# Performance work log

Measured on AMD Instinct MI355X. Metric: run time of the kernel, lower is better.

Reference implementation:

```python
import jax, jax.numpy as jnp
import numpy as np


def _layernorm(x, g, b, eps=1e-5):
    m = x.mean(-1, keepdims=True)
    v = ((x - m) ** 2).mean(-1, keepdims=True)
    return (x - m) * jax.lax.rsqrt(v + eps) * g + b


def _silu(x):
    return x * jax.nn.sigmoid(x)


def _mamba_mixer(x, in_w, conv_w, conv_b, xp_w, dt_w, dt_b, A_log, Dp, out_w):
    # x: (B, L, C) ; HF Mamba slow-path math
    B, L, C = x.shape
    dI = in_w.shape[0] // 2
    h, gate = jnp.split(x @ in_w.T, 2, axis=-1)  # (B, L, dI) each
    hc = jnp.transpose(h, (0, 2, 1))             # (B, dI, L)
    K = conv_w.shape[-1]
    hc = jax.lax.conv_general_dilated(hc, conv_w, (1,), [(K - 1, 0)],
                                      feature_group_count=dI,
                                      dimension_numbers=('NCH', 'OIH', 'NCH'))
    hc = _silu(hc + conv_b[None, :, None])
    u = jnp.transpose(hc, (0, 2, 1))             # (B, L, dI)
    R = dt_w.shape[1]
    N = A_log.shape[1]
    dt, Bs, Cs = jnp.split(u @ xp_w.T, [R, R + N], axis=-1)
    dt = jax.nn.softplus(dt @ dt_w.T + dt_b)     # (B, L, dI)
    A = -jnp.exp(A_log)                          # (dI, N)
    dA = jnp.exp(dt[..., None] * A)              # (B, L, dI, N)
    dBu = dt[..., None] * Bs[:, :, None, :] * u[..., None]  # (B, L, dI, N)

    def step(state, inp):
        dA_t, dBu_t, C_t = inp
        state = dA_t * state + dBu_t             # (B, dI, N)
        y = jnp.einsum('bdn,bn->bd', state, C_t)
        return state, y

    h0 = jnp.zeros((B, dI, N), x.dtype)
    _, ys = jax.lax.scan(step, h0, (jnp.swapaxes(dA, 0, 1),
                                    jnp.swapaxes(dBu, 0, 1),
                                    jnp.swapaxes(Cs, 0, 1)))
    y = jnp.swapaxes(ys, 0, 1)                   # (B, L, dI)
    y = (y + u * Dp) * _silu(gate)
    return y @ out_w.T


def _mixffn(x, H, W, fc1_w, fc1_b, pe_w, pe_b, fc2_w, fc2_b):
    B, L, C = x.shape
    img = jnp.transpose(x, (0, 2, 1)).reshape(B, C, H, W)
    t = jnp.einsum('bchw,fc->bfhw', img, fc1_w[:, :, 0, 0]) + fc1_b[None, :, None, None]
    Fch = pe_w.shape[0]
    t = jax.lax.conv_general_dilated(t, pe_w, (1, 1), [(1, 1), (1, 1)],
                                     feature_group_count=Fch,
                                     dimension_numbers=('NCHW', 'OIHW', 'NCHW'))
    t = t + pe_b[None, :, None, None]
    t = jax.nn.gelu(t, approximate=False)
    t = jnp.einsum('bfhw,cf->bchw', t, fc2_w[:, :, 0, 0]) + fc2_b[None, :, None, None]
    return jnp.transpose(t.reshape(B, C, L), (0, 2, 1))


def _forward(x, norm1_g, norm1_b, in_w, conv_w, conv_b, xp_w, dt_w, dt_b, A_log, Dp,
             out_w, norm2_g, norm2_b, gate_w, fc1_w, fc1_b, pe_w, pe_b, fc2_w, fc2_b,
             rand_index, H, W):
    identity = x
    B = x.shape[0]
    x_in = jnp.concatenate([x, jnp.flip(x, 1), x[:, rand_index]], axis=0)  # (3B, L, C)
    xn = _layernorm(x_in, norm1_g, norm1_b)
    y = _mamba_mixer(xn, in_w, conv_w, conv_b, xp_w, dt_w, dt_b, A_log, Dp, out_w)
    fwd, rev, shf = jnp.split(y, 3, axis=0)
    rev = jnp.flip(rev, 1)
    inv = jnp.argsort(rand_index)
    shf = shf[:, inv]
    g_in = jnp.concatenate([fwd.mean(1), rev.mean(1), shf.mean(1)], axis=-1)  # (B, 3C)
    g = jax.nn.softmax(g_in @ gate_w.T, axis=-1)                              # (B, 3)
    y = g[:, 0, None, None] * fwd + g[:, 1, None, None] * rev + g[:, 2, None, None] * shf
    x1 = identity + y
    xn2 = _layernorm(x1, norm2_g, norm2_b)
    return x1 + _mixffn(xn2, H, W, fc1_w, fc1_b, pe_w, pe_b, fc2_w, fc2_b)


def setup_inputs() -> dict:
    B, H, W, C = 2, 64, 64, 128
    L = H * W
    dI, N, K, R, Fch = 384, 4, 4, 128, 512
    key = jax.random.key(0)
    ks = jax.random.split(key, 32)
    s = lambda i, shape, sc=0.02: jax.random.normal(ks[i], shape, jnp.float32) * sc
    A_log = jnp.log(jnp.broadcast_to(jnp.arange(1, N + 1, dtype=jnp.float32), (dI, N)))
    return {
        'x': jax.random.normal(ks[0], (B, L, C), jnp.float32),
        'rand_index': jax.random.permutation(ks[1], L),
        'H': H, 'W': W,
        'norm1_g': jnp.ones((C,), jnp.float32),
        'norm1_b': jnp.zeros((C,), jnp.float32),
        'in_w': s(2, (2 * dI, C)),
        'conv_w': s(3, (dI, 1, K), 0.1),
        'conv_b': jnp.zeros((dI,), jnp.float32),
        'xp_w': s(4, (R + 2 * N, dI)),
        'dt_w': s(5, (dI, R)),
        'dt_b': s(6, (dI,), 0.1),
        'A_log': A_log,
        'Dp': jnp.ones((dI,), jnp.float32),
        'out_w': s(7, (C, dI)),
        'norm2_g': jnp.ones((C,), jnp.float32),
        'norm2_b': jnp.zeros((C,), jnp.float32),
        'gate_w': s(8, (3, 3 * C)),
        'fc1_w': s(9, (Fch, C, 1, 1)),
        'fc1_b': jnp.zeros((Fch,), jnp.float32),
        'pe_w': s(10, (Fch, 1, 3, 3), 0.1),
        'pe_b': jnp.zeros((Fch,), jnp.float32),
        'fc2_w': s(11, (C, Fch, 1, 1)),
        'fc2_b': jnp.zeros((C,), jnp.float32),
    }


def reference(x, rand_index, H, W, norm1_g, norm1_b, in_w, conv_w, conv_b, xp_w,
              dt_w, dt_b, A_log, Dp, out_w, norm2_g, norm2_b, gate_w,
              fc1_w, fc1_b, pe_w, pe_b, fc2_w, fc2_b):
    return _forward(x, norm1_g, norm1_b, in_w, conv_w, conv_b, xp_w, dt_w, dt_b,
                    A_log, Dp, out_w, norm2_g, norm2_b, gate_w, fc1_w, fc1_b,
                    pe_w, pe_b, fc2_w, fc2_b, rand_index, H, W)
```

## Files before the change

kernel.cpp:

```cpp
#include <hip/hip_runtime.h>
#include <math.h>

#define LLEN 4096
#define CCH 128
#define DI 384
#define NST 4
#define SBN 6
#define NB 2
#define FCH 512
#define NCHUNK 128
#define TSTEP 32

typedef short bf16x8 __attribute__((ext_vector_type(8)));
typedef short bf16x4 __attribute__((ext_vector_type(4)));
typedef float f32x4 __attribute__((ext_vector_type(4)));
typedef float f32x8 __attribute__((ext_vector_type(8)));

__device__ __forceinline__ float wave_sum(float v) {
#pragma unroll
    for (int o = 32; o > 0; o >>= 1) v += __shfl_xor(v, o);
    return v;
}

__device__ __forceinline__ short f2bf(float f) {
    unsigned int u = __float_as_uint(f);
    unsigned int r = (u + 0x7fffu + ((u >> 16) & 1u)) >> 16;
    return (short)r;
}
__device__ __forceinline__ float bf2f(short s) {
    return __uint_as_float(((unsigned int)(unsigned short)s) << 16);
}

#define OFF_IN  0
#define OFF_DTC 98304
#define OFF_BC  245760
#define OFF_OUT 248832
#define OFF_FC1 297984
#define OFF_FC2 363520
#define OFF_END 429056
#define NCONV   281600
#define NCBLK   1100
#define GWCBLK  14
#define LN1OFF  (NCBLK + 576 + GWCBLK + 16)
#define LN1BLK  2048

__global__ __launch_bounds__(256) void conv_comp(const float* __restrict__ in_w,
                                                 const float* __restrict__ xp_w,
                                                 const float* __restrict__ dt_w,
                                                 const float* __restrict__ out_w,
                                                 const float* __restrict__ fc1_w,
                                                 const float* __restrict__ fc2_w,
                                                 const float* __restrict__ gate_w,
                                                 const int* __restrict__ ridx,
                                                 const float* __restrict__ x,
                                                 const float* __restrict__ n1g,
                                                 const float* __restrict__ n1b,
                                                 short* __restrict__ wb,
                                                 float* __restrict__ colsum,
                                                 float* __restrict__ gwc,
                                                 int* __restrict__ inv,
                                                 short* __restrict__ xn)
{
    int bid = blockIdx.x;
    if (bid < NCBLK) {
        int i = bid * 256 + threadIdx.x;
        if (i >= NCONV) return;
        int idx = (i < OFF_DTC) ? i : i + (OFF_OUT - OFF_DTC);
        float v;
        if (idx < OFF_DTC)      v = in_w[idx];
        else if (idx < OFF_OUT) v = xp_w[128 * 384 + (idx - OFF_BC)];
        else if (idx < OFF_FC1) v = out_w[idx - OFF_OUT];
        else if (idx < OFF_FC2) v = fc1_w[idx - OFF_FC1];
        else                    v = fc2_w[idx - OFF_FC2];
        wb[idx] = f2bf(v);
    } else if (bid < NCBLK + 576) {
        if (bid == NCBLK) {
            for (int i = threadIdx.x; i < SBN * DI; i += 256) colsum[i] = 0.f;
        }
        int ji = (bid - NCBLK) * 256 + threadIdx.x;
        int j = ji / 384, k = ji % 384;
        float acc = 0.f;
#pragma unroll 8
        for (int n = 0; n < 128; n++)
            acc += dt_w[j * 128 + n] * xp_w[n * 384 + k];
        wb[OFF_DTC + j * 384 + k] = f2bf(acc);
    } else if (bid < NCBLK + 576 + GWCBLK) {
        int idx = (bid - NCBLK - 576) * 256 + threadIdx.x;
        if (idx >= 3456) return;
        int j = idx / 1152, rem = idx % 1152;
        int s = rem / 384, d = rem % 384;
        float acc = 0.f;
#pragma unroll 8
        for (int c = 0; c < 128; c++)
            acc += gate_w[j * 384 + s * 128 + c] * out_w[c * 384 + d];
        gwc[idx] = acc;
    } else if (bid < LN1OFF) {
        int l = (bid - NCBLK - 576 - GWCBLK) * 256 + threadIdx.x;
        if (l < LLEN) inv[ridx[l]] = l;
    } else {
        int r = (bid - LN1OFF) * 4 + (threadIdx.x >> 6);
        int lane = threadIdx.x & 63;
        const float* src = x + (size_t)r * CCH;
        float v0 = src[lane], v1 = src[lane + 64];
        float m = wave_sum(v0 + v1) * (1.f / 128.f);
        float d0 = v0 - m, d1 = v1 - m;
        float var = wave_sum(d0 * d0 + d1 * d1) * (1.f / 128.f);
        float rstd = rsqrtf(var + 1e-5f);
        short* dst = xn + (size_t)r * CCH;
        dst[lane]      = f2bf(d0 * rstd * n1g[lane]      + n1b[lane]);
        dst[lane + 64] = f2bf(d1 * rstd * n1g[lane + 64] + n1b[lane + 64]);
    }
}

template<int EPI>
__global__ __launch_bounds__(256) void gemm_w(const short* __restrict__ A, int lda,
                                              const short* __restrict__ W, int ldw,
                                              const float* __restrict__ bias,
                                              short* __restrict__ Cb, int ldc,
                                              int Kd)
{
    __shared__ short Als[64 * 72];
    __shared__ short Wls[128 * 72];
    int tid = threadIdx.x;
    int wid = tid >> 6, lane = tid & 63;
    int wm = wid >> 1, wn = wid & 1;
    int l15 = lane & 15, l4 = lane >> 4;
    int bm = blockIdx.x * 64, bn = blockIdx.y * 128;
    int srow = tid >> 3, scol = (tid & 7) * 8;
    f32x4 acc[2][4] = {};
    for (int k0 = 0; k0 < Kd; k0 += 64) {
        bf16x8 av0 = *(const bf16x8*)&A[(size_t)(bm + srow) * lda + k0 + scol];
        bf16x8 av1 = *(const bf16x8*)&A[(size_t)(bm + srow + 32) * lda + k0 + scol];
        bf16x8 wv[4];
#pragma unroll
        for (int q = 0; q < 4; q++)
            wv[q] = *(const bf16x8*)&W[(size_t)(bn + srow + 32 * q) * ldw + k0 + scol];
        __syncthreads();
        *(bf16x8*)&Als[srow * 72 + scol] = av0;
        *(bf16x8*)&Als[(srow + 32) * 72 + scol] = av1;
#pragma unroll
        for (int q = 0; q < 4; q++)
            *(bf16x8*)&Wls[(srow + 32 * q) * 72 + scol] = wv[q];
        __syncthreads();
#pragma unroll
        for (int ks = 0; ks < 2; ks++) {
            bf16x8 af[2], bw[4];
#pragma unroll
            for (int f = 0; f < 2; f++)
                af[f] = *(const bf16x8*)&Als[(wm * 32 + f * 16 + l15) * 72 + ks * 32 + l4 * 8];
#pragma unroll
            for (int j = 0; j < 4; j++)
                bw[j] = *(const bf16x8*)&Wls[(wn * 64 + j * 16 + l15) * 72 + ks * 32 + l4 * 8];
#pragma unroll
            for (int i = 0; i < 2; i++)
#pragma unroll
                for (int j = 0; j < 4; j++)
                    acc[i][j] = __builtin_amdgcn_mfma_f32_16x16x32_bf16(af[i], bw[j], acc[i][j], 0, 0, 0);
        }
    }
#pragma unroll
    for (int i = 0; i < 2; i++) {
        int row0 = bm + wm * 32 + i * 16 + l4 * 4;
#pragma unroll
        for (int j = 0; j < 4; j++) {
            int col = bn + wn * 64 + j * 16 + l15;
            float bv = (EPI == 6) ? bias[col] : 0.f;
#pragma unroll
            for (int r = 0; r < 4; r++)
                Cb[(size_t)(row0 + r) * ldc + col] = f2bf(acc[i][j][r] + bv);
        }
    }
}

__global__ __launch_bounds__(256) void gemm_bc(const short* __restrict__ A,
                                               const short* __restrict__ W,
                                               float* __restrict__ C0)
{
    __shared__ short Als[64 * 72];
    __shared__ short Wls[64 * 72];
    int tid = threadIdx.x;
    int wid = tid >> 6, lane = tid & 63;
    int wm = wid >> 1, wn = wid & 1;
    int l15 = lane & 15, l4 = lane >> 4;
    int bm = blockIdx.x * 64;
    int srow = tid >> 3, scol = (tid & 7) * 8;
    f32x4 acc[2][2] = {};
    for (int k0 = 0; k0 < DI; k0 += 64) {
        bf16x8 av0 = *(const bf16x8*)&A[(size_t)(bm + srow) * DI + k0 + scol];
        bf16x8 av1 = *(const bf16x8*)&A[(size_t)(bm + srow + 32) * DI + k0 + scol];
        bf16x8 wv0 = {};
        if (srow < 8) wv0 = *(const bf16x8*)&W[(size_t)srow * DI + k0 + scol];
        __syncthreads();
        *(bf16x8*)&Als[srow * 72 + scol] = av0;
        *(bf16x8*)&Als[(srow + 32) * 72 + scol] = av1;
        *(bf16x8*)&Wls[srow * 72 + scol] = wv0;
        if (srow >= 24) *(bf16x8*)&Wls[(srow + 32) * 72 + scol] = bf16x8{};
        else if (srow >= 8) *(bf16x8*)&Wls[srow * 72 + scol] = wv0;
        __syncthreads();
#pragma unroll
        for (int ks = 0; ks < 2; ks++) {
            bf16x8 af[2];
#pragma unroll
            for (int f = 0; f < 2; f++)
                af[f] = *(const bf16x8*)&Als[(wm * 32 + f * 16 + l15) * 72 + ks * 32 + l4 * 8];
            if (wn == 0) {
                bf16x8 bw = *(const bf16x8*)&Wls[(l15)*72 + ks * 32 + l4 * 8];
#pragma unroll
                for (int i = 0; i < 2; i++)
                    acc[i][0] = __builtin_amdgcn_mfma_f32_16x16x32_bf16(af[i], bw, acc[i][0], 0, 0, 0);
            }
        }
    }
    if (wn == 0 && l15 < 8) {
#pragma unroll
        for (int i = 0; i < 2; i++) {
            int row0 = bm + wm * 32 + i * 16 + l4 * 4;
#pragma unroll
            for (int r = 0; r < 4; r++)
                C0[(size_t)(row0 + r) * 8 + l15] = acc[i][0][r];
        }
    }
}

__global__ __launch_bounds__(256) void gemm_dt(const short* __restrict__ A,
                                               const short* __restrict__ W,
                                               const float* __restrict__ bias,
                                               short* __restrict__ Cb)
{
    __shared__ short Als[64 * 72];
    __shared__ short Wls[384 * 72];
    int tid = threadIdx.x;
    int wid = tid >> 6, lane = tid & 63;
    int wm = wid >> 1, wn = wid & 1;
    int l15 = lane & 15, l4 = lane >> 4;
    int bm = blockIdx.x * 64;
    int srow = tid >> 3, scol = (tid & 7) * 8;
    f32x4 acc[2][12] = {};
    for (int k0 = 0; k0 < 384; k0 += 64) {
        bf16x8 av0 = *(const bf16x8*)&A[(size_t)(bm + srow) * DI + k0 + scol];
        bf16x8 av1 = *(const bf16x8*)&A[(size_t)(bm + srow + 32) * DI + k0 + scol];
        bf16x8 wv[12];
#pragma unroll
        for (int q = 0; q < 12; q++)
            wv[q] = *(const bf16x8*)&W[(size_t)(srow + 32 * q) * DI + k0 + scol];
        __syncthreads();
        *(bf16x8*)&Als[srow * 72 + scol] = av0;
        *(bf16x8*)&Als[(srow + 32) * 72 + scol] = av1;
#pragma unroll
        for (int q = 0; q < 12; q++)
            *(bf16x8*)&Wls[(srow + 32 * q) * 72 + scol] = wv[q];
        __syncthreads();
#pragma unroll
        for (int ks = 0; ks < 2; ks++) {
            bf16x8 af[2];
#pragma unroll
            for (int f = 0; f < 2; f++)
                af[f] = *(const bf16x8*)&Als[(wm * 32 + f * 16 + l15) * 72 + ks * 32 + l4 * 8];
#pragma unroll
            for (int j = 0; j < 12; j++) {
                bf16x8 bw = *(const bf16x8*)&Wls[(wn * 192 + j * 16 + l15) * 72 + ks * 32 + l4 * 8];
#pragma unroll
                for (int i = 0; i < 2; i++)
                    acc[i][j] = __builtin_amdgcn_mfma_f32_16x16x32_bf16(af[i], bw, acc[i][j], 0, 0, 0);
            }
        }
    }
#pragma unroll
    for (int i = 0; i < 2; i++) {
        int row0 = bm + wm * 32 + i * 16 + l4 * 4;
#pragma unroll
        for (int j = 0; j < 12; j++) {
            int col = wn * 192 + j * 16 + l15;
            float bv = bias[col];
#pragma unroll
            for (int r = 0; r < 4; r++) {
                float v = acc[i][j][r] + bv;
                v = (v > 20.f) ? v : __logf(1.f + __expf(v));
                Cb[(size_t)(row0 + r) * DI + col] = f2bf(v);
            }
        }
    }
}

__global__ __launch_bounds__(192) void dwconv_silu_v3(const short* __restrict__ hg,
                                                      const int* __restrict__ ridx,
                                                      const float* __restrict__ cw,
                                                      const float* __restrict__ cb,
                                                      short* __restrict__ ub)
{
    int t = threadIdx.x;
    int c = t % 48, rs = t / 48;
    int blk = blockIdx.x;
    int sb = blk >> 7;
    int s = sb >> 1, bb = sb & 1;
    int l0 = ((blk & 127) << 5) + rs * 8;
    int d0 = c * 8;
    float w0[8], w1[8], w2[8], w3[8], bs[8];
#pragma unroll
    for (int e = 0; e < 8; e++) {
        int d = d0 + e;
        bs[e] = cb[d];
        w0[e] = cw[d * 4 + 0]; w1[e] = cw[d * 4 + 1];
        w2[e] = cw[d * 4 + 2]; w3[e] = cw[d * 4 + 3];
    }
    float r0[8], r1[8], r2[8];
#pragma unroll
    for (int e = 0; e < 8; e++) { r0[e] = 0.f; r1[e] = 0.f; r2[e] = 0.f; }
    if (l0 - 3 >= 0) {
        int j = l0 - 3;
        int sl = (s == 0) ? j : (s == 1 ? LLEN - 1 - j : ridx[j]);
        bf16x8 v = *(const bf16x8*)&hg[(size_t)(bb * LLEN + sl) * 768 + d0];
#pragma unroll
        for (int e = 0; e < 8; e++) r0[e] = bf2f(v[e]);
    }
    if (l0 - 2 >= 0) {
        int j = l0 - 2;
        int sl = (s == 0) ? j : (s == 1 ? LLEN - 1 - j : ridx[j]);
        bf16x8 v = *(const bf16x8*)&hg[(size_t)(bb * LLEN + sl) * 768 + d0];
#pragma unroll
        for (int e = 0; e < 8; e++) r1[e] = bf2f(v[e]);
    }
    if (l0 - 1 >= 0) {
        int j = l0 - 1;
        int sl = (s == 0) ? j : (s == 1 ? LLEN - 1 - j : ridx[j]);
        bf16x8 v = *(const bf16x8*)&hg[(size_t)(bb * LLEN + sl) * 768 + d0];
#pragma unroll
        for (int e = 0; e < 8; e++) r2[e] = bf2f(v[e]);
    }
#pragma unroll
    for (int i = 0; i < 8; i++) {
        int j = l0 + i;
        int sl = (s == 0) ? j : (s == 1 ? LLEN - 1 - j : ridx[j]);
        bf16x8 v = *(const bf16x8*)&hg[(size_t)(bb * LLEN + sl) * 768 + d0];
        float r3[8];
#pragma unroll
        for (int e = 0; e < 8; e++) r3[e] = bf2f(v[e]);
        bf16x8 ov;
#pragma unroll
        for (int e = 0; e < 8; e++) {
            float a = bs[e] + w0[e] * r0[e] + w1[e] * r1[e] + w2[e] * r2[e] + w3[e] * r3[e];
            ov[e] = f2bf(a * __builtin_amdgcn_rcpf(1.f + __expf(-a)));
        }
        *(bf16x8*)&ub[(size_t)(sb * LLEN + j) * DI + d0] = ov;
#pragma unroll
        for (int e = 0; e < 8; e++) { r0[e] = r1[e]; r1[e] = r2[e]; r2[e] = r3[e]; }
    }
}

__global__ __launch_bounds__(DI) void scan_phaseA2(const short* __restrict__ dtb,
                                                   const float* __restrict__ bc,
                                                   const short* __restrict__ ub,
                                                   const float* __restrict__ A_log,
                                                   float* __restrict__ PS)
{
    __shared__ short ds_dt[TSTEP * DI];
    __shared__ short ds_u[TSTEP * DI];
    __shared__ float ds_bc[TSTEP * 8];
    int tid = threadIdx.x;
    int bid = blockIdx.x;
    int sb = bid / NCHUNK, chunk = bid % NCHUNK;
    int base = sb * LLEN + chunk * TSTEP;
    {
        int rr = tid / 48, cc = (tid % 48) * 8;
#pragma unroll
        for (int p = 0; p < 4; p++) {
            int row = p * 8 + rr;
            *(bf16x8*)&ds_dt[row * DI + cc] = *(const bf16x8*)&dtb[(size_t)(base + row) * DI + cc];
            *(bf16x8*)&ds_u[row * DI + cc]  = *(const bf16x8*)&ub[(size_t)(base + row) * DI + cc];
        }
        if (tid < TSTEP * 8) ds_bc[tid] = bc[(size_t)base * 8 + tid];
    }
    int d = tid;
    f32x4 al = *(const f32x4*)&A_log[d * 4];
    float a[NST];
#pragma unroll
    for (int n = 0; n < NST; n++) a[n] = -__expf(al[n]);
    __syncthreads();
    float s[NST] = {0.f, 0.f, 0.f, 0.f}, p[NST] = {1.f, 1.f, 1.f, 1.f};
    for (int t = 0; t < TSTEP; t++) {
        float dtv = bf2f(ds_dt[t * DI + d]);
        float dtu = dtv * bf2f(ds_u[t * DI + d]);
#pragma unroll
        for (int n = 0; n < NST; n++) {
            float dA = __expf(dtv * a[n]);
            s[n] = dA * s[n] + dtu * ds_bc[t * 8 + n];
            p[n] *= dA;
        }
    }
    f32x8 v;
#pragma unroll
    for (int n = 0; n < NST; n++) { v[2 * n] = p[n]; v[2 * n + 1] = s[n]; }
    *(f32x8*)&PS[(size_t)(sb * NCHUNK + chunk) * 3072 + d * 8] = v;
}

__global__ __launch_bounds__(256) void scan_phaseB2(const float* __restrict__ PS,
                                                    float* __restrict__ I)
{
    int gid = blockIdx.x * 256 + threadIdx.x;
    if (gid >= SBN * 1536) return;
    int sb = gid / 1536, dn = gid % 1536;
    const float* ps = PS + (size_t)sb * NCHUNK * 3072 + dn * 2;
    float* Ip = I + (size_t)sb * NCHUNK * 1536 + dn;
    float st = 0.f;
    for (int c = 0; c < NCHUNK; c += 8) {
        float2 v[8];
#pragma unroll
        for (int q = 0; q < 8; q++) v[q] = *(const float2*)&ps[(size_t)(c + q) * 3072];
#pragma unroll
        for (int q = 0; q < 8; q++) { Ip[(size_t)(c + q) * 1536] = st; st = v[q].x * st + v[q].y; }
    }
}

__global__ __launch_bounds__(DI) void scan_phaseC3(const short* __restrict__ dtb,
                                                   const float* __restrict__ bc,
                                                   const short* __restrict__ ub,
                                                   const short* __restrict__ hg,
                                                   const int* __restrict__ ridx,
                                                   const float* __restrict__ A_log,
                                                   const float* __restrict__ Dp,
                                                   const float* __restrict__ I,
                                                   short* __restrict__ ymix,
                                                   float* __restrict__ colsum)
{
    __shared__ short ds_dt[TSTEP * DI];
    __shared__ short ds_u[TSTEP * DI];
    __shared__ float ds_bc[TSTEP * 8];
    __shared__ int ds_src[TSTEP];
    int tid = threadIdx.x;
    int bid = blockIdx.x;
    int sb = bid / NCHUNK, chunk = bid % NCHUNK;
    int s2 = sb >> 1, bb = sb & 1;
    int base = sb * LLEN + chunk * TSTEP;
    {
        int rr = tid / 48, cc = (tid % 48) * 8;
#pragma unroll
        for (int p = 0; p < 4; p++) {
            int row = p * 8 + rr;
            *(bf16x8*)&ds_dt[row * DI + cc] = *(const bf16x8*)&dtb[(size_t)(base + row) * DI + cc];
            *(bf16x8*)&ds_u[row * DI + cc]  = *(const bf16x8*)&ub[(size_t)(base + row) * DI + cc];
        }
        if (tid < TSTEP * 8) ds_bc[tid] = bc[(size_t)base * 8 + tid];
        if (tid < TSTEP) {
            int l = chunk * TSTEP + tid;
            int sl = (s2 == 0) ? l : (s2 == 1 ? LLEN - 1 - l : ridx[l]);
            ds_src[tid] = bb * LLEN + sl;
        }
    }
    int d = tid;
    f32x4 al = *(const f32x4*)&A_log[d * 4];
    float a[NST];
#pragma unroll
    for (int n = 0; n < NST; n++) a[n] = -__expf(al[n]);
    __syncthreads();
    float s[NST];
    {
        f32x4 si = *(const f32x4*)&I[(size_t)(sb * NCHUNK + chunk) * 1536 + d * 4];
#pragma unroll
        for (int n = 0; n < NST; n++) s[n] = si[n];
    }
    float Dv = Dp[d];
    float csum = 0.f;
    for (int t = 0; t < TSTEP; t++) {
        float dtv = bf2f(ds_dt[t * DI + d]);
        float uv = bf2f(ds_u[t * DI + d]);
        float dtu = dtv * uv;
        float y = 0.f;
#pragma unroll
        for (int n = 0; n < NST; n++) {
            float dA = __expf(dtv * a[n]);
            s[n] = dA * s[n] + dtu * ds_bc[t * 8 + n];
            y += s[n] * ds_bc[t * 8 + 4 + n];
        }
        float gt = bf2f(hg[(size_t)ds_src[t] * 768 + 384 + d]);
        float sg = gt * __builtin_amdgcn_rcpf(1.f + __expf(-gt));
        float val = (y + uv * Dv) * sg;
        ymix[(size_t)(base + t) * DI + d] = f2bf(val);
        csum += val;
    }
    atomicAdd(&colsum[sb * DI + d], csum);
}

__global__ __launch_bounds__(256) void combine_outproj_ln2(const short* __restrict__ ymix,
                                                           const float* __restrict__ x,
                                                           const float* __restrict__ colsum,
                                                           const float* __restrict__ gwc,
                                                           const int* __restrict__ inv,
                                                           const short* __restrict__ Wout,
                                                           const float* __restrict__ n2g,
                                                           const float* __restrict__ n2b,
                                                           float* __restrict__ x1,
                                                           short* __restrict__ xn2)
{
    __shared__ short Als[64 * 72];
    __shared__ short Wls[128 * 72];
    __shared__ float xs[64][132];
    __shared__ int ssrc[192];
    __shared__ float msh[64], rsh[64];
    __shared__ float part[4][3];
    __shared__ float gsh[3];
    int tid = threadIdx.x;
    int bm = blockIdx.x * 64;
    int bb = bm >> 12;
    if (tid < 64) {
        int l = (bm & 4095) + tid;
        ssrc[tid * 3 + 0] = bb * LLEN + l;
        ssrc[tid * 3 + 1] = (2 + bb) * LLEN + (LLEN - 1 - l);
        ssrc[tid * 3 + 2] = (4 + bb) * LLEN + inv[l];
    }
    int wid = tid >> 6, lane = tid & 63;
    {
        float a0 = 0.f, a1 = 0.f, a2 = 0.f;
        for (int i = tid; i < 1152; i += 256) {
            int s = i / 384, d = i % 384;
            float cv = colsum[(s * 2 + bb) * 384 + d];
            a0 += cv * gwc[i];
            a1 += cv * gwc[1152 + i];
            a2 += cv * gwc[2304 + i];
        }
        a0 = wave_sum(a0); a1 = wave_sum(a1); a2 = wave_sum(a2);
        if (lane == 0) { part[wid][0] = a0; part[wid][1] = a1; part[wid][2] = a2; }
    }
    __syncthreads();
    if (tid == 0) {
        float l0 = 0.f, l1 = 0.f, l2 = 0.f;
#pragma unroll
        for (int w = 0; w < 4; w++) { l0 += part[w][0]; l1 += part[w][1]; l2 += part[w][2]; }
        l0 *= (1.f / 4096.f); l1 *= (1.f / 4096.f); l2 *= (1.f / 4096.f);
        float mx = fmaxf(l0, fmaxf(l1, l2));
        float e0 = __expf(l0 - mx), e1 = __expf(l1 - mx), e2 = __expf(l2 - mx);
        float iv = __builtin_amdgcn_rcpf(e0 + e1 + e2);
        gsh[0] = e0 * iv; gsh[1] = e1 * iv; gsh[2] = e2 * iv;
    }
    __syncthreads();
    float g0 = gsh[0], g1 = gsh[1], g2 = gsh[2];
    int wm = wid >> 1, wn = wid & 1;
    int l15 = lane & 15, l4 = lane >> 4;
    int srow = tid >> 3, scol = (tid & 7) * 8;
    f32x4 acc[2][4] = {};
    for (int k0 = 0; k0 < DI; k0 += 64) {
        bf16x8 cmb[2];
#pragma unroll
        for (int hh = 0; hh < 2; hh++) {
            int r = srow + 32 * hh;
            bf16x8 vf = *(const bf16x8*)&ymix[(size_t)ssrc[r * 3 + 0] * DI + k0 + scol];
            bf16x8 vr = *(const bf16x8*)&ymix[(size_t)ssrc[r * 3 + 1] * DI + k0 + scol];
            bf16x8 vs = *(const bf16x8*)&ymix[(size_t)ssrc[r * 3 + 2] * DI + k0 + scol];
#pragma unroll
            for (int e = 0; e < 8; e++)
                cmb[hh][e] = f2bf(g0 * bf2f(vf[e]) + g1 * bf2f(vr[e]) + g2 * bf2f(vs[e]));
        }
        bf16x8 wv[4];
#pragma unroll
        for (int q = 0; q < 4; q++)
            wv[q] = *(const bf16x8*)&Wout[(size_t)(srow + 32 * q) * DI + k0 + scol];
        __syncthreads();
        *(bf16x8*)&Als[srow * 72 + scol] = cmb[0];
        *(bf16x8*)&Als[(srow + 32) * 72 + scol] = cmb[1];
#pragma unroll
        for (int q = 0; q < 4; q++)
            *(bf16x8*)&Wls[(srow + 32 * q) * 72 + scol] = wv[q];
        __syncthreads();
#pragma unroll
        for (int ks = 0; ks < 2; ks++) {
            bf16x8 af[2], bw[4];
#pragma unroll
            for (int f = 0; f < 2; f++)
                af[f] = *(const bf16x8*)&Als[(wm * 32 + f * 16 + l15) * 72 + ks * 32 + l4 * 8];
#pragma unroll
            for (int j = 0; j < 4; j++)
                bw[j] = *(const bf16x8*)&Wls[(wn * 64 + j * 16 + l15) * 72 + ks * 32 + l4 * 8];
#pragma unroll
            for (int i = 0; i < 2; i++)
#pragma unroll
                for (int j = 0; j < 4; j++)
                    acc[i][j] = __builtin_amdgcn_mfma_f32_16x16x32_bf16(af[i], bw[j], acc[i][j], 0, 0, 0);
        }
    }
#pragma unroll
    for (int i = 0; i < 2; i++) {
        int rowl = wm * 32 + i * 16 + l4 * 4;
#pragma unroll
        for (int j = 0; j < 4; j++) {
            int col = wn * 64 + j * 16 + l15;
#pragma unroll
            for (int r = 0; r < 4; r++)
                xs[rowl + r][col] = acc[i][j][r] + x[(size_t)(bm + rowl + r) * CCH + col];
        }
    }
    __syncthreads();
    {
        int row = tid >> 2, q = tid & 3;
        float sum = 0.f, sq = 0.f;
#pragma unroll
        for (int c = q * 32; c < q * 32 + 32; c++) { float v = xs[row][c]; sum += v; sq += v * v; }
        sum += __shfl_xor(sum, 1); sq += __shfl_xor(sq, 1);
        sum += __shfl_xor(sum, 2); sq += __shfl_xor(sq, 2);
        if (q == 0) {
            float m = sum * (1.f / 128.f);
            float var = sq * (1.f / 128.f) - m * m;
            msh[row] = m;
            rsh[row] = rsqrtf(fmaxf(var, 0.f) + 1e-5f);
        }
    }
    __syncthreads();
    {
        int col = tid & 127;
        float gg = n2g[col], b2 = n2b[col];
#pragma unroll
        for (int e = 0; e < 32; e++) {
            int row = e * 2 + (tid >> 7);
            float v = xs[row][col];
            x1[(size_t)(bm + row) * CCH + col] = v;
            xn2[(size_t)(bm + row) * CCH + col] = f2bf((v - msh[row]) * rsh[row] * gg + b2);
        }
    }
}

__global__ __launch_bounds__(256) void peconv_fc2(const short* __restrict__ t,
                                                  const float* __restrict__ pw,
                                                  const float* __restrict__ pb,
                                                  const short* __restrict__ W2,
                                                  const float* __restrict__ fc2_b,
                                                  const float* __restrict__ x1,
                                                  float* __restrict__ out)
{
    __shared__ short t2ls[32 * 520];
    __shared__ short Wls[128 * 72];
    int tid = threadIdx.x;
    int fc = tid & 127;
    int wsr = tid >> 7;
    int blk = blockIdx.x;
    int whalf = blk & 1, h = (blk >> 1) & 63, bb = blk >> 7;
    int w0 = whalf * 32 + wsr * 16;
    int f0 = fc * 4;
    {
        float wt[9][4], bias4[4];
#pragma unroll
        for (int e = 0; e < 4; e++) {
            bias4[e] = pb[f0 + e];
#pragma unroll
            for (int k = 0; k < 9; k++) wt[k][e] = pw[(f0 + e) * 9 + k];
        }
        size_t base = (size_t)bb * 4096 * FCH;
        float cm1[3][4], cc[3][4], cn[3][4];
#pragma unroll
        for (int rr = 0; rr < 3; rr++)
#pragma unroll
            for (int e = 0; e < 4; e++) { cm1[rr][e] = 0.f; cc[rr][e] = 0.f; }
#pragma unroll
        for (int rr = 0; rr < 3; rr++) {
            int hh = h + rr - 1;
            if (hh >= 0 && hh < 64) {
                if (w0 - 1 >= 0) {
                    bf16x4 v = *(const bf16x4*)&t[base + ((size_t)hh * 64 + (w0 - 1)) * FCH + f0];
#pragma unroll
                    for (int e = 0; e < 4; e++) cm1[rr][e] = bf2f(v[e]);
                }
                bf16x4 v = *(const bf16x4*)&t[base + ((size_t)hh * 64 + w0) * FCH + f0];
#pragma unroll
                for (int e = 0; e < 4; e++) cc[rr][e] = bf2f(v[e]);
            }
        }
#pragma unroll
        for (int i = 0; i < 16; i++) {
            int w = w0 + i;
#pragma unroll
            for (int rr = 0; rr < 3; rr++) {
#pragma unroll
                for (int e = 0; e < 4; e++) cn[rr][e] = 0.f;
                int hh = h + rr - 1;
                if (hh >= 0 && hh < 64 && w + 1 < 64) {
                    bf16x4 v = *(const bf16x4*)&t[base + ((size_t)hh * 64 + (w + 1)) * FCH + f0];
#pragma unroll
                    for (int e = 0; e < 4; e++) cn[rr][e] = bf2f(v[e]);
                }
            }
            bf16x4 ov;
#pragma unroll
            for (int e = 0; e < 4; e++) {
                float acc = bias4[e];
#pragma unroll
                for (int rr = 0; rr < 3; rr++) {
                    acc += wt[rr * 3 + 0][e] * cm1[rr][e];
                    acc += wt[rr * 3 + 1][e] * cc[rr][e];
                    acc += wt[rr * 3 + 2][e] * cn[rr][e];
                }
                ov[e] = f2bf(0.5f * acc * (1.f + erff(acc * 0.70710678118654752f)));
            }
            int pix = wsr * 16 + i;
            *(bf16x4*)&t2ls[pix * 520 + f0] = ov;
#pragma unroll
            for (int rr = 0; rr < 3; rr++)
#pragma unroll
                for (int e = 0; e < 4; e++) { cm1[rr][e] = cc[rr][e]; cc[rr][e] = cn[rr][e]; }
        }
    }
    __syncthreads();
    int wid = tid >> 6, lane = tid & 63;
    int wm = wid >> 1, wn = wid & 1;
    int l15 = lane & 15, l4 = lane >> 4;
    int srow = tid >> 3, scol = (tid & 7) * 8;
    int bm = bb * 4096 + h * 64 + whalf * 32;
    f32x4 acc[4] = {};
    for (int k0 = 0; k0 < FCH; k0 += 64) {
        bf16x8 wv[4];
#pragma unroll
        for (int q = 0; q < 4; q++)
            wv[q] = *(const bf16x8*)&W2[(size_t)(srow + 32 * q) * FCH + k0 + scol];
        __syncthreads();
#pragma unroll
        for (int q = 0; q < 4; q++)
            *(bf16x8*)&Wls[(srow + 32 * q) * 72 + scol] = wv[q];
        __syncthreads();
#pragma unroll
        for (int ks = 0; ks < 2; ks++) {
            bf16x8 af = *(const bf16x8*)&t2ls[(wm * 16 + l15) * 520 + k0 + ks * 32 + l4 * 8];
#pragma unroll
            for (int j = 0; j < 4; j++) {
                bf16x8 bw = *(const bf16x8*)&Wls[(wn * 64 + j * 16 + l15) * 72 + ks * 32 + l4 * 8];
                acc[j] = __builtin_amdgcn_mfma_f32_16x16x32_bf16(af, bw, acc[j], 0, 0, 0);
            }
        }
    }
#pragma unroll
    for (int j = 0; j < 4; j++) {
        int col = wn * 64 + j * 16 + l15;
        float bv = fc2_b[col];
#pragma unroll
        for (int r = 0; r < 4; r++) {
            int row = bm + wm * 16 + l4 * 4 + r;
            out[(size_t)row * CCH + col] = acc[j][r] + bv + x1[(size_t)row * CCH + col];
        }
    }
}

extern "C" void kernel_launch(void* const* d_in, const int* in_sizes, int n_in,
                              void* d_out, int out_size, void* d_ws, size_t ws_size,
                              hipStream_t stream)
{
    (void)in_sizes; (void)n_in; (void)ws_size; (void)out_size;
    const float* x      = (const float*)d_in[0];
    const int*   ridx   = (const int*)d_in[1];
    const float* n1g    = (const float*)d_in[4];
    const float* n1b    = (const float*)d_in[5];
    const float* in_w   = (const float*)d_in[6];
    const float* conv_w = (const float*)d_in[7];
    const float* conv_b = (const float*)d_in[8];
    const float* xp_w   = (const float*)d_in[9];
    const float* dt_w   = (const float*)d_in[10];
    const float* dt_b   = (const float*)d_in[11];
    const float* A_log  = (const float*)d_in[12];
    const float* Dp     = (const float*)d_in[13];
    const float* out_w  = (const float*)d_in[14];
    const float* n2g    = (const float*)d_in[15];
    const float* n2b    = (const float*)d_in[16];
    const float* gate_w = (const float*)d_in[17];
    const float* fc1_w  = (const float*)d_in[18];
    const float* fc1_b  = (const float*)d_in[19];
    const float* pe_w   = (const float*)d_in[20];
    const float* pe_b   = (const float*)d_in[21];
    const float* fc2_w  = (const float*)d_in[22];
    const float* fc2_b  = (const float*)d_in[23];
    float* out = (float*)d_out;

    float* ws = (float*)d_ws;
    short* wb   = (short*)ws;
    float* regA = ws + 215040;
    float* regB = regA + 2097152;
    float* regC = regB + 9437184;
    float* regD = regC + 4718592;
    float* regE = regD + 4718592;
    float* regF = regE + 4718592;
    float* regG = regF + 2359296;
    float* smallb = regG + 196608;

    short* xn   = (short*)regA;
    float* Ibuf = regA;
    short* tbuf = (short*)regA;
    short* hg   = (short*)regB;
    float* x1   = regB + 3145728;
    short* xn2  = (short*)(regB + 4194304);
    short* ub   = (short*)regC;
    short* ymix = (short*)regD;
    short* dtb  = (short*)regE;
    float* PS   = regF;
    float* xpbc = regG;
    float* colsum = smallb;
    float* gwcb   = smallb + 2304;
    float* gbuf   = gwcb + 3456;
    int*   invb   = (int*)(gbuf + 8);
    (void)gbuf;

    const int M6 = SBN * LLEN;
    const int M2 = NB * LLEN;

    conv_comp<<<LN1OFF + LN1BLK, 256, 0, stream>>>(in_w, xp_w, dt_w, out_w, fc1_w, fc2_w,
                                                   gate_w, ridx, x, n1g, n1b,
                                                   wb, colsum, gwcb, invb, xn);
    gemm_w<5><<<dim3(M2 / 64, 6), 256, 0, stream>>>(xn, CCH, wb + OFF_IN, CCH, nullptr, hg, 768, CCH);
    dwconv_silu_v3<<<768, 192, 0, stream>>>(hg, ridx, conv_w, conv_b, ub);
    gemm_bc<<<M6 / 64, 256, 0, stream>>>(ub, wb + OFF_BC, xpbc);
    gemm_dt<<<M6 / 64, 256, 0, stream>>>(ub, wb + OFF_DTC, dt_b, dtb);
    scan_phaseA2<<<SBN * NCHUNK, DI, 0, stream>>>(dtb, xpbc, ub, A_log, PS);
    scan_phaseB2<<<36, 256, 0, stream>>>(PS, Ibuf);
    scan_phaseC3<<<SBN * NCHUNK, DI, 0, stream>>>(dtb, xpbc, ub, hg, ridx, A_log, Dp, Ibuf, ymix, colsum);
    combine_outproj_ln2<<<M2 / 64, 256, 0, stream>>>(ymix, x, colsum, gwcb, invb, wb + OFF_OUT, n2g, n2b, x1, xn2);
    gemm_w<6><<<dim3(M2 / 64, 4), 256, 0, stream>>>(xn2, CCH, wb + OFF_FC1, CCH, fc1_b, tbuf, FCH, CCH);
    peconv_fc2<<<256, 256, 0, stream>>>(tbuf, pe_w, pe_b, wb + OFF_FC2, fc2_b, x1, out);
}
```

Baseline: 172.7 us.

## Fuse dt and B/C projections into one GEMM; fuse fc1 into out-proj/LN2 kernel

The separate gemm_bc and gemm_dt kernels become a single gemm_dtbc. It reads the ub activation once and handles the 8 B/C columns as an extra 16-column MFMA tile on the wn==1 waves. It assumes the B/C weight rows sit directly after the dt weight rows at OFF_DTC+384*DI. The fc1 GEMM is also folded into combine_outproj_ln2: the LN2 output is staged in shared memory and multiplied by W1 in-kernel, so the xn2 round trip and two launches go away. In exchange, the merged projection kernel uses more shared memory and registers, and the combine kernel now runs four serial 128-column fc1 tiles with only 128 blocks, which may lower parallelism.

Measured after the change: 170.7 us. No clear change (-1.2%).

```diff
diff --git a/kernel.cpp b/kernel.cpp
--- a/kernel.cpp
+++ b/kernel.cpp
@@ -172,70 +172,21 @@
     }
 }
 
-__global__ __launch_bounds__(256) void gemm_bc(const short* __restrict__ A,
-                                               const short* __restrict__ W,
-                                               float* __restrict__ C0)
+__global__ __launch_bounds__(256) void gemm_dtbc(const short* __restrict__ A,
+                                                 const short* __restrict__ W,
+                                                 const float* __restrict__ bias,
+                                                 short* __restrict__ Cb,
+                                                 float* __restrict__ bcout)
 {
     __shared__ short Als[64 * 72];
-    __shared__ short Wls[64 * 72];
+    __shared__ short Wls[400 * 72];
     int tid = threadIdx.x;
     int wid = tid >> 6, lane = tid & 63;
     int wm = wid >> 1, wn = wid & 1;
     int l15 = lane & 15, l4 = lane >> 4;
     int bm = blockIdx.x * 64;
     int srow = tid >> 3, scol = (tid & 7) * 8;
-    f32x4 acc[2][2] = {};
-    for (int k0 = 0; k0 < DI; k0 += 64) {
-        bf16x8 av0 = *(const bf16x8*)&A[(size_t)(bm + srow) * DI + k0 + scol];
-        bf16x8 av1 = *(const bf16x8*)&A[(size_t)(bm + srow + 32) * DI + k0 + scol];
-        bf16x8 wv0 = {};
-        if (srow < 8) wv0 = *(const bf16x8*)&W[(size_t)srow * DI + k0 + scol];
-        __syncthreads();
-        *(bf16x8*)&Als[srow * 72 + scol] = av0;
-        *(bf16x8*)&Als[(srow + 32) * 72 + scol] = av1;
-        *(bf16x8*)&Wls[srow * 72 + scol] = wv0;
-        if (srow >= 24) *(bf16x8*)&Wls[(srow + 32) * 72 + scol] = bf16x8{};
-        else if (srow >= 8) *(bf16x8*)&Wls[srow * 72 + scol] = wv0;
-        __syncthreads();
-#pragma unroll
-        for (int ks = 0; ks < 2; ks++) {
-            bf16x8 af[2];
-#pragma unroll
-            for (int f = 0; f < 2; f++)
-                af[f] = *(const bf16x8*)&Als[(wm * 32 + f * 16 + l15) * 72 + ks * 32 + l4 * 8];
-            if (wn == 0) {
-                bf16x8 bw = *(const bf16x8*)&Wls[(l15)*72 + ks * 32 + l4 * 8];
-#pragma unroll
-                for (int i = 0; i < 2; i++)
-                    acc[i][0] = __builtin_amdgcn_mfma_f32_16x16x32_bf16(af[i], bw, acc[i][0], 0, 0, 0);
-            }
-        }
-    }
-    if (wn == 0 && l15 < 8) {
-#pragma unroll
-        for (int i = 0; i < 2; i++) {
-            int row0 = bm + wm * 32 + i * 16 + l4 * 4;
-#pragma unroll
-            for (int r = 0; r < 4; r++)
-                C0[(size_t)(row0 + r) * 8 + l15] = acc[i][0][r];
-        }
-    }
-}
-
-__global__ __launch_bounds__(256) void gemm_dt(const short* __restrict__ A,
-                                               const short* __restrict__ W,
-                                               const float* __restrict__ bias,
-                                               short* __restrict__ Cb)
-{
-    __shared__ short Als[64 * 72];
-    __shared__ short Wls[384 * 72];
-    int tid = threadIdx.x;
-    int wid = tid >> 6, lane = tid & 63;
-    int wm = wid >> 1, wn = wid & 1;
-    int l15 = lane & 15, l4 = lane >> 4;
-    int bm = blockIdx.x * 64;
-    int srow = tid >> 3, scol = (tid & 7) * 8;
-    f32x4 acc[2][12] = {};
+    f32x4 acc[2][13] = {};
     for (int k0 = 0; k0 < 384; k0 += 64) {
         bf16x8 av0 = *(const bf16x8*)&A[(size_t)(bm + srow) * DI + k0 + scol];
         bf16x8 av1 = *(const bf16x8*)&A[(size_t)(bm + srow + 32) * DI + k0 + scol];
@@ -243,12 +194,16 @@
 #pragma unroll
         for (int q = 0; q < 12; q++)
             wv[q] = *(const bf16x8*)&W[(size_t)(srow + 32 * q) * DI + k0 + scol];
+        bf16x8 wbc = {};
+        if (srow < 8) wbc = *(const bf16x8*)&W[(size_t)(384 + srow) * DI + k0 + scol];
         __syncthreads();
         *(bf16x8*)&Als[srow * 72 + scol] = av0;
         *(bf16x8*)&Als[(srow + 32) * 72 + scol] = av1;
 #pragma unroll
         for (int q = 0; q < 12; q++)
             *(bf16x8*)&Wls[(srow + 32 * q) * 72 + scol] = wv[q];
+        if (srow < 16)
+            *(bf16x8*)&Wls[(384 + srow) * 72 + scol] = wbc;
         __syncthreads();
 #pragma unroll
         for (int ks = 0; ks < 2; ks++) {
@@ -262,6 +217,12 @@
 #pragma unroll
                 for (int i = 0; i < 2; i++)
                     acc[i][j] = __builtin_amdgcn_mfma_f32_16x16x32_bf16(af[i], bw, acc[i][j], 0, 0, 0);
+            }
+            if (wn == 1) {
+                bf16x8 bw = *(const bf16x8*)&Wls[(384 + l15) * 72 + ks * 32 + l4 * 8];
+#pragma unroll
+                for (int i = 0; i < 2; i++)
+                    acc[i][12] = __builtin_amdgcn_mfma_f32_16x16x32_bf16(af[i], bw, acc[i][12], 0, 0, 0);
             }
         }
     }
@@ -278,6 +239,11 @@
                 v = (v > 20.f) ? v : __logf(1.f + __expf(v));
                 Cb[(size_t)(row0 + r) * DI + col] = f2bf(v);
             }
+        }
+        if (wn == 1 && l15 < 8) {
+#pragma unroll
+            for (int r = 0; r < 4; r++)
+                bcout[(size_t)(row0 + r) * 8 + l15] = acc[i][12][r];
         }
     }
 }
@@ -488,8 +454,10 @@
                                                            const short* __restrict__ Wout,
                                                            const float* __restrict__ n2g,
                                                            const float* __restrict__ n2b,
+                                                           const short* __restrict__ W1,
+                                                           const float* __restrict__ fc1_b,
                                                            float* __restrict__ x1,
-                                                           short* __restrict__ xn2)
+                                                           short* __restrict__ tbuf)
 {
     __shared__ short Als[64 * 72];
     __shared__ short Wls[128 * 72];
@@ -498,6 +466,7 @@
     __shared__ float msh[64], rsh[64];
     __shared__ float part[4][3];
     __shared__ float gsh[3];
+    short* xnls = (short*)xs;
     int tid = threadIdx.x;
     int bm = blockIdx.x * 64;
     int bb = bm >> 12;
@@ -603,6 +572,7 @@
         }
     }
     __syncthreads();
+    short sval[32];
     {
         int col = tid & 127;
         float gg = n2g[col], b2 = n2b[col];
@@ -611,7 +581,58 @@
             int row = e * 2 + (tid >> 7);
             float v = xs[row][col];
             x1[(size_t)(bm + row) * CCH + col] = v;
-            xn2[(size_t)(bm + row) * CCH + col] = f2bf((v - msh[row]) * rsh[row] * gg + b2);
+            sval[e] = f2bf((v - msh[row]) * rsh[row] * gg + b2);
+        }
+    }
+    __syncthreads();
+    {
+        int col = tid & 127;
+#pragma unroll
+        for (int e = 0; e < 32; e++) {
+            int row = e * 2 + (tid >> 7);
+            xnls[row * 136 + col] = sval[e];
+        }
+    }
+    __syncthreads();
+    for (int bn = 0; bn < FCH; bn += 128) {
+        f32x4 acc1[2][4] = {};
+        for (int k0 = 0; k0 < CCH; k0 += 64) {
+            bf16x8 wv[4];
+#pragma unroll
+            for (int q = 0; q < 4; q++)
+                wv[q] = *(const bf16x8*)&W1[(size_t)(bn + srow + 32 * q) * CCH + k0 + scol];
+            __syncthreads();
+#pragma unroll
+            for (int q = 0; q < 4; q++)
+                *(bf16x8*)&Wls[(srow + 32 * q) * 72 + scol] = wv[q];
+            __syncthreads();
+#pragma unroll
+            for (int ks = 0; ks < 2; ks++) {
+                bf16x8 af[2], bw[4];
+#pragma unroll
+                for (int f = 0; f < 2; f++)
+                    af[f] = *(const bf16x8*)&xnls[(wm * 32 + f * 16 + l15) * 136 + k0 + ks * 32 + l4 * 8];
+#pragma unroll
+                for (int j = 0; j < 4; j++)
+                    bw[j] = *(const bf16x8*)&Wls[(wn * 64 + j * 16 + l15) * 72 + ks * 32 + l4 * 8];
+#pragma unroll
+                for (int i = 0; i < 2; i++)
+#pragma unroll
+                    for (int j = 0; j < 4; j++)
+                        acc1[i][j] = __builtin_amdgcn_mfma_f32_16x16x32_bf16(af[i], bw[j], acc1[i][j], 0, 0, 0);
+            }
+        }
+#pragma unroll
+        for (int i = 0; i < 2; i++) {
+            int row0 = bm + wm * 32 + i * 16 + l4 * 4;
+#pragma unroll
+            for (int j = 0; j < 4; j++) {
+                int col = bn + wn * 64 + j * 16 + l15;
+                float bv = fc1_b[col];
+#pragma unroll
+                for (int r = 0; r < 4; r++)
+                    tbuf[(size_t)(row0 + r) * FCH + col] = f2bf(acc1[i][j][r] + bv);
+            }
         }
     }
 }
@@ -779,7 +800,6 @@
     short* tbuf = (short*)regA;
     short* hg   = (short*)regB;
     float* x1   = regB + 3145728;
-    short* xn2  = (short*)(regB + 4194304);
     short* ub   = (short*)regC;
     short* ymix = (short*)regD;
     short* dtb  = (short*)regE;
@@ -787,9 +807,7 @@
     float* xpbc = regG;
     float* colsum = smallb;
     float* gwcb   = smallb + 2304;
-    float* gbuf   = gwcb + 3456;
-    int*   invb   = (int*)(gbuf + 8);
-    (void)gbuf;
+    int*   invb   = (int*)(gwcb + 3456 + 8);
 
     const int M6 = SBN * LLEN;
     const int M2 = NB * LLEN;
@@ -799,12 +817,11 @@
                                                    wb, colsum, gwcb, invb, xn);
     gemm_w<5><<<dim3(M2 / 64, 6), 256, 0, stream>>>(xn, CCH, wb + OFF_IN, CCH, nullptr, hg, 768, CCH);
     dwconv_silu_v3<<<768, 192, 0, stream>>>(hg, ridx, conv_w, conv_b, ub);
-    gemm_bc<<<M6 / 64, 256, 0, stream>>>(ub, wb + OFF_BC, xpbc);
-    gemm_dt<<<M6 / 64, 256, 0, stream>>>(ub, wb + OFF_DTC, dt_b, dtb);
+    gemm_dtbc<<<M6 / 64, 256, 0, stream>>>(ub, wb + OFF_DTC, dt_b, dtb, xpbc);
     scan_phaseA2<<<SBN * NCHUNK, DI, 0, stream>>>(dtb, xpbc, ub, A_log, PS);
     scan_phaseB2<<<36, 256, 0, stream>>>(PS, Ibuf);
     scan_phaseC3<<<SBN * NCHUNK, DI, 0, stream>>>(dtb, xpbc, ub, hg, ridx, A_log, Dp, Ibuf, ymix, colsum);
-    combine_outproj_ln2<<<M2 / 64, 256, 0, stream>>>(ymix, x, colsum, gwcb, invb, wb + OFF_OUT, n2g, n2b, x1, xn2);
-    gemm_w<6><<<dim3(M2 / 64, 4), 256, 0, stream>>>(xn2, CCH, wb + OFF_FC1, CCH, fc1_b, tbuf, FCH, CCH);
+    combine_outproj_ln2<<<M2 / 64, 256, 0, stream>>>(ymix, x, colsum, gwcb, invb, wb + OFF_OUT,
+                                                     n2g, n2b, wb + OFF_FC1, fc1_b, x1, tbuf);
     peconv_fc2<<<256, 256, 0, stream>>>(tbuf, pe_w, pe_b, wb + OFF_FC2, fc2_b, x1, out);
 }
```
